# Kernel tuning notes

Measured on AMD Instinct MI355X. Metric: run time of the kernel, lower is better.

Reference implementation:

```python
import jax, jax.numpy as jnp
import numpy as np

N_NUM = 2048      # recurrent neurons (== input_num)
E_NUM = 1638
OUT_NUM = 512     # readout size
TIME_CONST = 0.1  # LIF leak


def setup_inputs() -> dict:
    key = jax.random.key(0)
    k1, k2, k3, k4, k5 = jax.random.split(key, 5)
    B = 4096
    return {
        "i_": jax.random.normal(k1, (B, N_NUM), dtype=jnp.float32),
        "x": jax.random.normal(k2, (B, N_NUM), dtype=jnp.float32),
        "r": jax.random.normal(k3, (N_NUM, N_NUM), dtype=jnp.float32) * (1.0 / np.sqrt(N_NUM)),
        "f": jax.random.normal(k4, (N_NUM, OUT_NUM), dtype=jnp.float32) * (1.0 / np.sqrt(N_NUM)),
        "b": jax.random.normal(k5, (N_NUM,), dtype=jnp.float32) * 0.01,
    }


def reference(i_, x, r, f, b):
    # EI sign vector: ei_mask is a diagonal matrix diag(signs); mm(ei_mask, A) == signs[:, None] * A
    signs = jnp.where(jnp.arange(N_NUM) < E_NUM, 1.0, -1.0).astype(i_.dtype)
    self_mask = 1.0 - jnp.eye(N_NUM, dtype=i_.dtype)  # no_self: zero diagonal

    # LIF state update: x <- (1 - tau) * x + tau * (i_ + b)   (noise_coeff = 0)
    x_new = (1.0 - TIME_CONST) * x + TIME_CONST * (i_ + b)
    u = jax.nn.relu(x_new)

    # Dale's law + self-mask on recurrent weights; Dale on feedforward weights
    r_eff = signs[:, None] * jnp.abs(r * self_mask)   # [N, N]
    f_eff = signs[:, None] * jnp.abs(f)               # [N, OUT]

    f_out = u @ f_eff   # [B, OUT]
    r_out = u @ r_eff   # [B, N]
    return (f_out, r_out, u)
```

## Files before the change

### kernel.cpp

```cpp
#include <hip/hip_runtime.h>
#include <hip/hip_bf16.h>

#define B_NUM 4096
#define N_NUM 2048
#define E_NUM 1638
#define OUT_NUM 512
#define NTOT 2560

typedef unsigned short u16;
typedef __attribute__((ext_vector_type(8))) __bf16 bf16x8;
typedef __attribute__((ext_vector_type(4))) float f32x4;

__device__ __forceinline__ u16 f2bf(float f) {
  union { float f; unsigned u; } v; v.f = f;
  unsigned r = v.u + 0x7fffu + ((v.u >> 16) & 1u);
  return (u16)(r >> 16);
}

__device__ __forceinline__ void gload_lds16(const u16* src, u16* dst) {
  __builtin_amdgcn_global_load_lds((__attribute__((address_space(1))) void*)src,
                                   (__attribute__((address_space(3))) void*)dst,
                                   16, 0, 0);
}

__global__ __launch_bounds__(256) void prep_u(const float* __restrict__ in_i,
                                              const float* __restrict__ in_x,
                                              const float* __restrict__ bias,
                                              float* __restrict__ u_f32,
                                              u16* __restrict__ u_bf16) {
  const int t = blockIdx.x * 256 + threadIdx.x;
  const int e = t * 4;
  const float4 iv = *(const float4*)(in_i + e);
  const float4 xv = *(const float4*)(in_x + e);
  const float4 bv = *(const float4*)(bias + (e & (N_NUM - 1)));
  float4 u;
  u.x = fmaxf(0.f, 0.9f * xv.x + 0.1f * (iv.x + bv.x));
  u.y = fmaxf(0.f, 0.9f * xv.y + 0.1f * (iv.y + bv.y));
  u.z = fmaxf(0.f, 0.9f * xv.z + 0.1f * (iv.z + bv.z));
  u.w = fmaxf(0.f, 0.9f * xv.w + 0.1f * (iv.w + bv.w));
  *(float4*)(u_f32 + e) = u;
  ushort4 ub;
  ub.x = f2bf(u.x); ub.y = f2bf(u.y); ub.z = f2bf(u.z); ub.w = f2bf(u.w);
  *(ushort4*)(u_bf16 + e) = ub;
}

__global__ __launch_bounds__(256) void prep_w(const float* __restrict__ r,
                                              const float* __restrict__ f,
                                              u16* __restrict__ wt) {
  __shared__ u16 ldsT[64][72];
  const int k0 = blockIdx.y * 64;
  const int n0 = blockIdx.x * 64;
  const int tid = threadIdx.x;
  const int rloc = tid >> 4;
  const int c4 = (tid & 15) * 4;
#pragma unroll
  for (int rr = 0; rr < 4; ++rr) {
    const int kl = rr * 16 + rloc;
    const int k = k0 + kl;
    const float sign = (k < E_NUM) ? 1.f : -1.f;
    float4 v;
    if (n0 < N_NUM) {
      v = *(const float4*)(r + k * N_NUM + n0 + c4);
    } else {
      v = *(const float4*)(f + k * OUT_NUM + (n0 - N_NUM) + c4);
    }
    float vals[4] = {v.x, v.y, v.z, v.w};
#pragma unroll
    for (int j = 0; j < 4; ++j) {
      float val = sign * fabsf(vals[j]);
      if (n0 < N_NUM && (n0 + c4 + j) == k) val = 0.f;
      ldsT[c4 + j][kl] = f2bf(val);
    }
  }
  __syncthreads();
  const int nl = tid >> 2;
  const int kc = (tid & 3) * 16;
  u16* dst = wt + (n0 + nl) * N_NUM + k0 + kc;
  *(uint4*)(dst) = *(const uint4*)&ldsT[nl][kc];
  *(uint4*)(dst + 8) = *(const uint4*)&ldsT[nl][kc + 8];
}

__global__ __launch_bounds__(256) void gemm_fused(const u16* __restrict__ U,
                                                  const u16* __restrict__ Wt,
                                                  float* __restrict__ out) {
  __shared__ u16 lA[128 * 64];
  __shared__ u16 lB[128 * 64];
  const int tid = threadIdx.x;
  const int wid = tid >> 6;
  const int lane = tid & 63;
  const int row0 = blockIdx.y * 128;
  const int col0 = blockIdx.x * 128;
  const int wr = (wid >> 1) * 64;
  const int wc = (wid & 1) * 64;

  f32x4 acc[4][4] = {};

  const int s_row = lane >> 3;
  const int s_col = (lane & 7) * 8;

  for (int k0 = 0; k0 < N_NUM; k0 += 64) {
#pragma unroll
    for (int i = 0; i < 4; ++i) {
      const int chunk = wid * 4 + i;
      gload_lds16(U + (row0 + chunk * 8 + s_row) * N_NUM + k0 + s_col,
                  &lA[chunk * 512]);
    }
#pragma unroll
    for (int i = 0; i < 4; ++i) {
      const int chunk = wid * 4 + i;
      gload_lds16(Wt + (col0 + chunk * 8 + s_row) * N_NUM + k0 + s_col,
                  &lB[chunk * 512]);
    }
    __syncthreads();

    const int lr = lane & 15;
#pragma unroll
    for (int kk = 0; kk < 64; kk += 32) {
      const int lc = kk + (lane >> 4) * 8;
      bf16x8 af[4], bfr[4];
#pragma unroll
      for (int mi = 0; mi < 4; ++mi)
        af[mi] = *(const bf16x8*)&lA[(wr + mi * 16 + lr) * 64 + lc];
#pragma unroll
      for (int ni = 0; ni < 4; ++ni)
        bfr[ni] = *(const bf16x8*)&lB[(wc + ni * 16 + lr) * 64 + lc];
#pragma unroll
      for (int mi = 0; mi < 4; ++mi)
#pragma unroll
        for (int ni = 0; ni < 4; ++ni)
          acc[mi][ni] = __builtin_amdgcn_mfma_f32_16x16x32_bf16(
              af[mi], bfr[ni], acc[mi][ni], 0, 0, 0);
    }
    __syncthreads();
  }

  const int orow = row0 + wr + ((lane >> 4) << 2);
  const int ocol = col0 + wc + (lane & 15);
#pragma unroll
  for (int mi = 0; mi < 4; ++mi) {
#pragma unroll
    for (int ni = 0; ni < 4; ++ni) {
      const int col = ocol + ni * 16;
#pragma unroll
      for (int q = 0; q < 4; ++q) {
        const int row = orow + mi * 16 + q;
        if (col < N_NUM)
          out[B_NUM * OUT_NUM + row * N_NUM + col] = acc[mi][ni][q];
        else
          out[row * OUT_NUM + (col - N_NUM)] = acc[mi][ni][q];
      }
    }
  }
}

extern "C" void kernel_launch(void* const* d_in, const int* in_sizes, int n_in,
                              void* d_out, int out_size, void* d_ws, size_t ws_size,
                              hipStream_t stream) {
  const float* i_ = (const float*)d_in[0];
  const float* x  = (const float*)d_in[1];
  const float* r  = (const float*)d_in[2];
  const float* f  = (const float*)d_in[3];
  const float* b  = (const float*)d_in[4];
  float* out = (float*)d_out;

  u16* U  = (u16*)d_ws;
  u16* Wt = (u16*)((char*)d_ws + (size_t)B_NUM * N_NUM * 2);

  float* u_region = out + (size_t)B_NUM * OUT_NUM + (size_t)B_NUM * N_NUM;

  prep_u<<<(B_NUM * N_NUM / 4) / 256, 256, 0, stream>>>(i_, x, b, u_region, U);
  prep_w<<<dim3(NTOT / 64, N_NUM / 64), 256, 0, stream>>>(r, f, Wt);
  gemm_fused<<<dim3(NTOT / 128, B_NUM / 128), 256, 0, stream>>>(U, Wt, out);
}
```

Baseline: 236.4 us.

## Replace GEMM with 256x256 double-buffered swizzled LDS pipeline kernel

Replaces the 128x128 single-buffered GEMM with a 512-thread 256x256 tile kernel that double-buffers A and B in LDS, prefetching the next k-tile while MFMAs run. LDS rows are XOR-swizzled to reduce bank conflicts, and barriers plus s_setprio interleave loads with compute. The larger tile cuts global traffic per flop but yields only 160 workgroups, fewer than the CU count, and uses far more LDS and registers per block.

```diff
diff --git a/kernel.cpp b/kernel.cpp
--- a/kernel.cpp
+++ b/kernel.cpp
@@ -6,6 +6,8 @@
 #define E_NUM 1638
 #define OUT_NUM 512
 #define NTOT 2560
+#define KDIM 2048
+#define NKT 32
 
 typedef unsigned short u16;
 typedef __attribute__((ext_vector_type(8))) __bf16 bf16x8;
@@ -17,11 +19,15 @@
   return (u16)(r >> 16);
 }
 
-__device__ __forceinline__ void gload_lds16(const u16* src, u16* dst) {
+__device__ __forceinline__ void gload16(const u16* src, u16* dst) {
   __builtin_amdgcn_global_load_lds((__attribute__((address_space(1))) void*)src,
                                    (__attribute__((address_space(3))) void*)dst,
                                    16, 0, 0);
 }
+
+#define BAR() do { asm volatile("" ::: "memory"); \
+                   __builtin_amdgcn_s_barrier();  \
+                   asm volatile("" ::: "memory"); } while (0)
 
 __global__ __launch_bounds__(256) void prep_u(const float* __restrict__ in_i,
                                               const float* __restrict__ in_x,
@@ -59,11 +65,8 @@
     const int k = k0 + kl;
     const float sign = (k < E_NUM) ? 1.f : -1.f;
     float4 v;
-    if (n0 < N_NUM) {
-      v = *(const float4*)(r + k * N_NUM + n0 + c4);
-    } else {
-      v = *(const float4*)(f + k * OUT_NUM + (n0 - N_NUM) + c4);
-    }
+    if (n0 < N_NUM) v = *(const float4*)(r + k * N_NUM + n0 + c4);
+    else            v = *(const float4*)(f + k * OUT_NUM + (n0 - N_NUM) + c4);
     float vals[4] = {v.x, v.y, v.z, v.w};
 #pragma unroll
     for (int j = 0; j < 4; ++j) {
@@ -75,82 +78,123 @@
   __syncthreads();
   const int nl = tid >> 2;
   const int kc = (tid & 3) * 16;
-  u16* dst = wt + (n0 + nl) * N_NUM + k0 + kc;
+  u16* dst = wt + (n0 + nl) * KDIM + k0 + kc;
   *(uint4*)(dst) = *(const uint4*)&ldsT[nl][kc];
   *(uint4*)(dst + 8) = *(const uint4*)&ldsT[nl][kc + 8];
 }
 
-__global__ __launch_bounds__(256) void gemm_fused(const u16* __restrict__ U,
-                                                  const u16* __restrict__ Wt,
-                                                  float* __restrict__ out) {
-  __shared__ u16 lA[128 * 64];
-  __shared__ u16 lB[128 * 64];
-  const int tid = threadIdx.x;
-  const int wid = tid >> 6;
-  const int lane = tid & 63;
-  const int row0 = blockIdx.y * 128;
-  const int col0 = blockIdx.x * 128;
-  const int wr = (wid >> 1) * 64;
-  const int wc = (wid & 1) * 64;
-
-  f32x4 acc[4][4] = {};
-
-  const int s_row = lane >> 3;
-  const int s_col = (lane & 7) * 8;
-
-  for (int k0 = 0; k0 < N_NUM; k0 += 64) {
-#pragma unroll
-    for (int i = 0; i < 4; ++i) {
-      const int chunk = wid * 4 + i;
-      gload_lds16(U + (row0 + chunk * 8 + s_row) * N_NUM + k0 + s_col,
-                  &lA[chunk * 512]);
-    }
-#pragma unroll
-    for (int i = 0; i < 4; ++i) {
-      const int chunk = wid * 4 + i;
-      gload_lds16(Wt + (col0 + chunk * 8 + s_row) * N_NUM + k0 + s_col,
-                  &lB[chunk * 512]);
-    }
-    __syncthreads();
-
-    const int lr = lane & 15;
-#pragma unroll
-    for (int kk = 0; kk < 64; kk += 32) {
-      const int lc = kk + (lane >> 4) * 8;
-      bf16x8 af[4], bfr[4];
-#pragma unroll
-      for (int mi = 0; mi < 4; ++mi)
-        af[mi] = *(const bf16x8*)&lA[(wr + mi * 16 + lr) * 64 + lc];
+__global__ __launch_bounds__(512, 2) void gemm8(const u16* __restrict__ U,
+                                                const u16* __restrict__ Wt,
+                                                float* __restrict__ out) {
+  __shared__ u16 lds[2][2][256 * 64];
+  const int t = threadIdx.x;
+  const int w = t >> 6, lane = t & 63;
+  const int lr = lane & 15, lg = lane >> 4;
+  const int wm = w >> 2, wn = w & 3;
+  const int row0 = blockIdx.y * 256;
+  const int col0 = blockIdx.x * 256;
+
+  const int srow = t >> 3;
+  const int koff = 8 * ((t & 7) ^ (srow & 7));
+  const u16* aS = U  + (row0 + srow) * KDIM + koff;
+  const u16* bS = Wt + (col0 + srow) * KDIM + koff;
+  const int stBase = (w * 8) * 64;
+
+  const int arow = wm * 128 + lr;
+  const int brow = wn * 64 + lr;
+  const int xs = (lr & 7) << 4;
+  const int ca0 = ((lg * 16) ^ xs) >> 1;
+  const int ca1 = ((64 + lg * 16) ^ xs) >> 1;
+
+  f32x4 acc[8][4] = {};
+
+#define STAGE_A(c, kt) { const int k0_ = (kt) * 64;                         \
+  _Pragma("unroll") for (int i_ = 0; i_ < 4; ++i_)                          \
+    gload16(aS + i_ * 64 * KDIM + k0_, &lds[c][0][i_ * 4096 + stBase]); }
+#define STAGE_B(c, kt) { const int k0_ = (kt) * 64;                         \
+  _Pragma("unroll") for (int i_ = 0; i_ < 4; ++i_)                          \
+    gload16(bS + i_ * 64 * KDIM + k0_, &lds[c][1][i_ * 4096 + stBase]); }
+
+  STAGE_B(0, 0);
+  STAGE_A(0, 0);
+  STAGE_B(1, 1);
+  asm volatile("s_waitcnt vmcnt(4)" ::: "memory");
+  __builtin_amdgcn_sched_barrier(0);
+  BAR();
+
+  for (int T = 0; T < NKT; ++T) {
+    const int c = T & 1;
+    const u16* lA = lds[c][0];
+    const u16* lB = lds[c][1];
+    bf16x8 bf[4][2], af[4][2];
+#pragma unroll
+    for (int ni = 0; ni < 4; ++ni) {
+      bf[ni][0] = *(const bf16x8*)&lB[(brow + ni * 16) * 64 + ca0];
+      bf[ni][1] = *(const bf16x8*)&lB[(brow + ni * 16) * 64 + ca1];
+    }
+#pragma unroll
+    for (int mi = 0; mi < 4; ++mi) {
+      af[mi][0] = *(const bf16x8*)&lA[(arow + mi * 16) * 64 + ca0];
+      af[mi][1] = *(const bf16x8*)&lA[(arow + mi * 16) * 64 + ca1];
+    }
+    { const int tn = (T + 1 < NKT) ? T + 1 : NKT - 1;
+      STAGE_A(c ^ 1, tn); }
+    BAR();
+    __builtin_amdgcn_s_setprio(1);
+#pragma unroll
+    for (int mi = 0; mi < 4; ++mi)
+#pragma unroll
+      for (int ni = 0; ni < 4; ++ni) {
+        acc[mi][ni] = __builtin_amdgcn_mfma_f32_16x16x32_bf16(af[mi][0], bf[ni][0], acc[mi][ni], 0, 0, 0);
+        acc[mi][ni] = __builtin_amdgcn_mfma_f32_16x16x32_bf16(af[mi][1], bf[ni][1], acc[mi][ni], 0, 0, 0);
+      }
+    __builtin_amdgcn_s_setprio(0);
+    BAR();
+#pragma unroll
+    for (int mi = 0; mi < 4; ++mi) {
+      af[mi][0] = *(const bf16x8*)&lA[(arow + 64 + mi * 16) * 64 + ca0];
+      af[mi][1] = *(const bf16x8*)&lA[(arow + 64 + mi * 16) * 64 + ca1];
+    }
+    { const int tn = (T + 2 < NKT) ? T + 2 : NKT - 1;
+      STAGE_B(c, tn); }
+    BAR();
+    __builtin_amdgcn_s_setprio(1);
+#pragma unroll
+    for (int mi = 0; mi < 4; ++mi)
+#pragma unroll
+      for (int ni = 0; ni < 4; ++ni) {
+        acc[4 + mi][ni] = __builtin_amdgcn_mfma_f32_16x16x32_bf16(af[mi][0], bf[ni][0], acc[4 + mi][ni], 0, 0, 0);
+        acc[4 + mi][ni] = __builtin_amdgcn_mfma_f32_16x16x32_bf16(af[mi][1], bf[ni][1], acc[4 + mi][ni], 0, 0, 0);
+      }
+    __builtin_amdgcn_s_setprio(0);
+    asm volatile("s_waitcnt vmcnt(4)" ::: "memory");
+    __builtin_amdgcn_sched_barrier(0);
+    BAR();
+  }
+  asm volatile("s_waitcnt vmcnt(0)" ::: "memory");
+
+  const int orow = row0 + wm * 128 + lg * 4;
+  const int ocol = col0 + wn * 64 + lr;
+  if (col0 < N_NUM) {
+    float* ro = out + B_NUM * OUT_NUM;
+#pragma unroll
+    for (int mi = 0; mi < 8; ++mi)
 #pragma unroll
       for (int ni = 0; ni < 4; ++ni)
-        bfr[ni] = *(const bf16x8*)&lB[(wc + ni * 16 + lr) * 64 + lc];
-#pragma unroll
-      for (int mi = 0; mi < 4; ++mi)
-#pragma unroll
-        for (int ni = 0; ni < 4; ++ni)
-          acc[mi][ni] = __builtin_amdgcn_mfma_f32_16x16x32_bf16(
-              af[mi], bfr[ni], acc[mi][ni], 0, 0, 0);
-    }
-    __syncthreads();
+#pragma unroll
+        for (int q = 0; q < 4; ++q)
+          ro[(orow + mi * 16 + q) * N_NUM + ocol + ni * 16] = acc[mi][ni][q];
+  } else {
+#pragma unroll
+    for (int mi = 0; mi < 8; ++mi)
+#pragma unroll
+      for (int ni = 0; ni < 4; ++ni)
+#pragma unroll
+        for (int q = 0; q < 4; ++q)
+          out[(orow + mi * 16 + q) * OUT_NUM + (ocol - N_NUM) + ni * 16] = acc[mi][ni][q];
   }
-
-  const int orow = row0 + wr + ((lane >> 4) << 2);
-  const int ocol = col0 + wc + (lane & 15);
-#pragma unroll
-  for (int mi = 0; mi < 4; ++mi) {
-#pragma unroll
-    for (int ni = 0; ni < 4; ++ni) {
-      const int col = ocol + ni * 16;
-#pragma unroll
-      for (int q = 0; q < 4; ++q) {
-        const int row = orow + mi * 16 + q;
-        if (col < N_NUM)
-          out[B_NUM * OUT_NUM + row * N_NUM + col] = acc[mi][ni][q];
-        else
-          out[row * OUT_NUM + (col - N_NUM)] = acc[mi][ni][q];
-      }
-    }
-  }
+#undef STAGE_A
+#undef STAGE_B
 }
 
 extern "C" void kernel_launch(void* const* d_in, const int* in_sizes, int n_in,
@@ -164,11 +208,11 @@
   float* out = (float*)d_out;
 
   u16* U  = (u16*)d_ws;
-  u16* Wt = (u16*)((char*)d_ws + (size_t)B_NUM * N_NUM * 2);
+  u16* Wt = (u16*)((char*)d_ws + (size_t)B_NUM * KDIM * 2);
 
   float* u_region = out + (size_t)B_NUM * OUT_NUM + (size_t)B_NUM * N_NUM;
 
   prep_u<<<(B_NUM * N_NUM / 4) / 256, 256, 0, stream>>>(i_, x, b, u_region, U);
   prep_w<<<dim3(NTOT / 64, N_NUM / 64), 256, 0, stream>>>(r, f, Wt);
-  gemm_fused<<<dim3(NTOT / 128, B_NUM / 128), 256, 0, stream>>>(U, Wt, out);
-}
+  gemm8<<<dim3(NTOT / 256, B_NUM / 256), 512, 0, stream>>>(U, Wt, out);
+}
```

Result: faster. 204.3 us (-13.6%).
